# Kernel optimization log

Measured on AMD Instinct MI355X. Metric: run time of the kernel, lower is better.

## Reference

```python
import jax, jax.numpy as jnp
import numpy as np

B, H, W, D, L, M = 16, 256, 256, 32, 4, 12  # batch, grid H, grid W, d_model, num_layers, modes
BN_EPS = 1e-5


def setup_inputs() -> dict:
    key = jax.random.key(0)
    ks = jax.random.split(key, 12)
    scale = 1.0 / (D * D)  # SpectralConv2d init scale: 1/(in_ch*out_ch)
    return {
        "x": jax.random.normal(ks[0], (B, H, W), jnp.float32),
        "coords_x": jax.random.uniform(ks[1], (1, 2, 1, H, W), dtype=jnp.float32),
        # linear_in: 3 -> D
        "w_in": jax.random.normal(ks[2], (D, 3), jnp.float32) * 0.3,
        "b_in": jnp.zeros((D,), jnp.float32),
        # per-layer spectral weights (real/imag), torch.rand-style uniform [0,1)*scale
        "w1r": jax.random.uniform(ks[3], (L, D, D, M, M), dtype=jnp.float32) * scale,
        "w1i": jax.random.uniform(ks[4], (L, D, D, M, M), dtype=jnp.float32) * scale,
        "w2r": jax.random.uniform(ks[5], (L, D, D, M, M), dtype=jnp.float32) * scale,
        "w2i": jax.random.uniform(ks[6], (L, D, D, M, M), dtype=jnp.float32) * scale,
        # per-layer pointwise linear D -> D
        "lw": jax.random.normal(ks[7], (L, D, D), jnp.float32) * (1.0 / np.sqrt(D)),
        "lb": jnp.zeros((L, D), jnp.float32),
        # per-layer BatchNorm affine params
        "gamma": jnp.ones((L, D), jnp.float32),
        "beta": jnp.zeros((L, D), jnp.float32),
        # linear_out: D -> 1
        "w_out": jax.random.normal(ks[8], (1, D), jnp.float32) * (1.0 / np.sqrt(D)),
        "b_out": jnp.zeros((1,), jnp.float32),
    }


def _fourier_layer(h, w1, w2, lw, lb, gamma, beta):
    # h: [B, D, H, W]
    Bh, C, Hh, Wh = h.shape
    h_ft = jnp.fft.rfft2(h)  # [B, D, H, W//2+1] complex64
    # low-mode truncation + complex channel mixing on two corner blocks
    top = jnp.einsum('bixy,ioxy->boxy', h_ft[:, :, :M, :M], w1)
    bot = jnp.einsum('bixy,ioxy->boxy', h_ft[:, :, Hh - M:, :M], w2)
    out_ft = jnp.zeros((Bh, C, Hh, Wh // 2 + 1), jnp.complex64)
    out_ft = out_ft.at[:, :, :M, :M].set(top).at[:, :, Hh - M:, :M].set(bot)
    y = jnp.fft.irfft2(out_ft, s=(Hh, Wh))  # [B, D, H, W]
    # residual pointwise linear (x + Linear(x)), then ReLU, then BatchNorm2d (batch stats)
    y = y + jnp.einsum('bchw,oc->bohw', y, lw) + lb[None, :, None, None]
    y = jax.nn.relu(y)
    mean = y.mean(axis=(0, 2, 3), keepdims=True)
    var = y.var(axis=(0, 2, 3), keepdims=True)
    y = (y - mean) * jax.lax.rsqrt(var + BN_EPS)
    return y * gamma[None, :, None, None] + beta[None, :, None, None]


def reference(x, coords_x, w_in, b_in, w1r, w1i, w2r, w2i, lw, lb, gamma, beta, w_out, b_out):
    # coords_x: [1,2,1,H,W] -> squeeze dim 2 -> broadcast to [B,2,H,W]
    cx = jnp.broadcast_to(coords_x[:, :, 0], (x.shape[0], 2, H, W))
    h = jnp.concatenate([x[:, None], cx], axis=1)  # [B, 3, H, W]
    h = jnp.einsum('bchw,dc->bdhw', h, w_in) + b_in[None, :, None, None]  # linear_in
    for i in range(L):  # fixed small layer count
        h = _fourier_layer(h, w1r[i] + 1j * w1i[i], w2r[i] + 1j * w2i[i],
                           lw[i], lb[i], gamma[i], beta[i])
    out = jnp.einsum('bdhw,od->bohw', h, w_out) + b_out[None, :, None, None]  # linear_out
    return out[:, 0]  # [B, H, W]
```

## Files before the change

### kernel.cpp

```cpp
#include <hip/hip_runtime.h>

constexpr double PI2 = 6.283185307179586476925286766559;
constexpr float INV_HW = 1.0f / 65536.0f;


__global__ __launch_bounds__(256) void k_init(float* __restrict__ cs,
                                              float* __restrict__ Tg) {
  int t = threadIdx.x;
  double a = PI2 * (double)t / 256.0;
  cs[2*t]   = (float)cos(a);
  cs[2*t+1] = (float)sin(a);
  for (int i = t; i < 1536; i += 256) {
    int k = i >> 7, xs = i & 127;
    double ang = PI2 * (double)(k * xs) / 256.0;
    Tg[i]        = (float)cos(ang);
    Tg[1536 + i] = (float)sin(ang);
  }
  for (int i = t; i < 176; i += 256) {
    int k = (i >> 4) + 1, j = i & 15;
    double ang = PI2 * (double)(k * j) / 256.0;
    Tg[3072 + i] = (float)cos(ang);
    Tg[3248 + i] = (float)sin(ang);
  }
}

__global__ __launch_bounds__(256) void k_prep(
    const float* __restrict__ w1r, const float* __restrict__ w1i,
    const float* __restrict__ w2r, const float* __restrict__ w2i,
    const float* __restrict__ lw, float* __restrict__ wf)
{
  const int bid = blockIdx.x;
  const int l = bid / 288, m = bid % 288;
  const int ky = m / 12, kx = m % 12;
  const int kyp = (ky < 12) ? ky : ky - 12;
  const float* wr_ = ((ky < 12) ? w1r : w2r) + l*147456;
  const float* wi_ = ((ky < 12) ? w1i : w2i) + l*147456;
  __shared__ float wre[1024], wim[1024], lwl[1024];
  const int tid = threadIdx.x;
  for (int f = tid; f < 1024; f += 256) {
    int idx = f*144 + kyp*12 + kx;
    wre[f] = wr_[idx]; wim[f] = wi_[idx];
    lwl[f] = lw[l*1024 + f];
  }
  __syncthreads();
  float* o_ = wf + (long)bid*2048;
  for (int f = tid; f < 1024; f += 256) {
    int i = f >> 5, o = f & 31;
    float ar = wre[f], ai = wim[f];
    #pragma unroll
    for (int c = 0; c < 32; ++c) {
      float lv = lwl[o*32 + c];
      ar += wre[i*32 + c] * lv;
      ai += wim[i*32 + c] * lv;
    }
    o_[f] = ar; o_[1024 + f] = ai;
  }
}

__global__ __launch_bounds__(256) void k_embed_fwd(
    const float* __restrict__ xin, const float* __restrict__ coords,
    const float* __restrict__ w_in, const float* __restrict__ b_in,
    const float* __restrict__ Tg, float* __restrict__ gxo)
{
  __shared__ float wl[96], bl[32];
  __shared__ __align__(16) float Tl[3168];
  __shared__ __align__(16) float E[32*132];
  __shared__ __align__(16) float O[32*132];
  const int tid = threadIdx.x;
  if (tid < 96) wl[tid] = w_in[tid];
  if (tid >= 96 && tid < 128) bl[tid-96] = b_in[tid-96];
  for (int i = tid; i < 1536; i += 256) {
    int k = i >> 7, xs0 = i & 127;
    Tl[k*132 + xs0]        = Tg[i];
    Tl[1584 + k*132 + xs0] = Tg[1536 + i];
  }
  const int b = blockIdx.x >> 8, y = blockIdx.x & 255;
  const int xs = tid & 127, half = tid >> 7;
  const int cbase = half << 4;
  const int xhi = (256 - xs) & 255;
  const float xvL = xin[(b*256 + y)*256 + xs];
  const float c0L = coords[y*256 + xs];
  const float c1L = coords[65536 + y*256 + xs];
  const float xvH = xin[(b*256 + y)*256 + xhi];
  const float c0H = coords[y*256 + xhi];
  const float c1H = coords[65536 + y*256 + xhi];
  __syncthreads();
  #pragma unroll
  for (int cc = 0; cc < 16; ++cc) {
    const int c = cbase + cc;
    float lo = wl[3*c]*xvL + wl[3*c+1]*c0L + wl[3*c+2]*c1L + bl[c];
    float hi = wl[3*c]*xvH + wl[3*c+1]*c0H + wl[3*c+2]*c1H + bl[c];
    E[c*132 + xs] = (xs == 0) ? lo : (lo + hi);
    O[c*132 + xs] = (xs == 0) ? 0.f : (lo - hi);
  }
  if (tid < 32) {
    const int c = tid;
    const float xv = xin[(b*256 + y)*256 + 128];
    const float c0 = coords[y*256 + 128];
    const float c1 = coords[65536 + y*256 + 128];
    E[c*132 + 128] = wl[3*c]*xv + wl[3*c+1]*c0 + wl[3*c+2]*c1 + bl[c];
  }
  __syncthreads();
  const int wv = tid >> 6, lane = tid & 63;
  const int seg = lane >> 3, chl = lane & 7;
  const int ch = wv*8 + chl;
  float ar[12], ai[12];
  #pragma unroll
  for (int k = 0; k < 12; ++k) { ar[k] = 0.f; ai[k] = 0.f; }
  {
    const float* Erow = &E[ch*132 + seg*16];
    const float* Orow = &O[ch*132 + seg*16];
    #pragma unroll
    for (int c4 = 0; c4 < 4; ++c4) {
      float4 E4 = *(const float4*)(Erow + 4*c4);
      float4 O4 = *(const float4*)(Orow + 4*c4);
      ar[0] += E4.x + E4.y + E4.z + E4.w;
      #pragma unroll
      for (int k = 1; k < 12; ++k) {
        float4 Tc4 = *(const float4*)&Tl[k*132 + seg*16 + 4*c4];
        float4 Ts4 = *(const float4*)&Tl[1584 + k*132 + seg*16 + 4*c4];
        ar[k] += E4.x*Tc4.x + E4.y*Tc4.y + E4.z*Tc4.z + E4.w*Tc4.w;
        ai[k] -= O4.x*Ts4.x + O4.y*Ts4.y + O4.z*Ts4.z + O4.w*Ts4.w;
      }
    }
  }
  #pragma unroll
  for (int k = 0; k < 12; ++k) {
    ar[k] += __shfl_xor(ar[k], 8, 64);
    ar[k] += __shfl_xor(ar[k], 16, 64);
    ar[k] += __shfl_xor(ar[k], 32, 64);
  }
  #pragma unroll
  for (int k = 1; k < 12; ++k) {
    ai[k] += __shfl_xor(ai[k], 8, 64);
    ai[k] += __shfl_xor(ai[k], 16, 64);
    ai[k] += __shfl_xor(ai[k], 32, 64);
  }
  {
    const float e128 = E[ch*132 + 128];
    float* gp = gxo + ((long)(b*256 + y)*32 + ch)*24;
    #pragma unroll
    for (int j = 0; j < 3; ++j) {
      const int v = seg*3 + j;
      if (v < 12) {
        float s = ar[v] + ((v & 1) ? -e128 : e128);
        gp[2*v] = s;
        if (v == 0) gp[1] = 0.f;
      } else if (v < 23) {
        gp[2*(v - 11) + 1] = ai[v - 11];
      }
    }
  }
}

__global__ __launch_bounds__(512) void k_spec(
    const float* __restrict__ gx, const float* __restrict__ cs,
    const float* __restrict__ bnp, const float* __restrict__ wfl,
    float* __restrict__ gy)
{
  const int bid = (blockIdx.x % 8) * 24 + blockIdx.x / 8;
  const int b = bid / 12, kx = bid % 12;
  __shared__ float2 Z[32*257];
  __shared__ float fcl[24*66];
  __shared__ float fml[24*66];
  __shared__ __align__(16) float csl[512];
  const int tid = threadIdx.x;
  if (tid < 512) csl[tid] = cs[tid];
  {
    const int ch = tid & 31;
    float sc = 1.0f, badd = 0.0f;
    if (bnp) { sc = bnp[ch]; if (kx == 0) badd = 256.0f * bnp[32 + ch]; }
    const float* src = gx + ((long)(b*256)*32 + ch)*24 + 2*kx;
    const int ybase = tid >> 5;
    #pragma unroll
    for (int i = 0; i < 16; ++i) {
      int y = ybase + 16*i;
      float2 v = *(const float2*)(src + (long)y*768);
      float2 w; w.x = sc*v.x + badd; w.y = sc*v.y;
      Z[ch*257 + y] = w;
    }
  }
  __syncthreads();
  for (int t = tid; t < 832; t += 512) {
    const int hf = t & 1, r = t >> 1;
    const int pr = r % 13, ch = r / 13;
    const int kyv = (pr <= 10) ? (pr + 1) : ((pr == 11) ? 0 : 244);
    const int y0 = hf << 7;
    int tt = (kyv * y0) & 255;
    float A = 0.f, Bv = 0.f, C2 = 0.f, D = 0.f;
    const float2* Zp = &Z[ch*257 + y0];
    for (int i = 0; i < 128; ++i) {
      float2 v = Zp[i];
      float2 w = *(const float2*)&csl[2*tt];
      A  += v.x*w.x;  D  += v.x*w.y;
      C2 += v.y*w.x;  Bv += v.y*w.y;
      tt = (tt + kyv) & 255;
    }
    A  += __shfl_xor(A, 1, 64);
    Bv += __shfl_xor(Bv, 1, 64);
    C2 += __shfl_xor(C2, 1, 64);
    D  += __shfl_xor(D, 1, 64);
    if (hf == 0) {
      const int slo = (pr <= 10) ? (pr + 1) : ((pr == 11) ? 0 : 12);
      fcl[slo*66 + 2*ch]     = A + Bv;
      fcl[slo*66 + 2*ch + 1] = C2 - D;
      if (pr <= 10) {
        fcl[(23 - pr)*66 + 2*ch]     = A - Bv;
        fcl[(23 - pr)*66 + 2*ch + 1] = C2 + D;
      }
    }
  }
  __syncthreads();
  for (int t = tid; t < 768; t += 512) {
    const int ky = t >> 5, o = t & 31;
    const float* wb = wfl + ((long)(ky*12 + kx))*2048;
    const float* fr = &fcl[ky*66];
    float ar = 0.f, ai = 0.f;
    #pragma unroll
    for (int i = 0; i < 32; ++i) {
      float fre = fr[2*i], fim = fr[2*i+1];
      float wr = wb[i*32 + o], wi = wb[1024 + i*32 + o];
      ar += fre*wr - fim*wi;
      ai += fre*wi + fim*wr;
    }
    fml[ky*66 + 2*o]     = ar;
    fml[ky*66 + 2*o + 1] = ai;
  }
  __syncthreads();
  {
    const int yp = tid & 127, og = tid >> 7;
    float tc[24], tsn[24];
    #pragma unroll
    for (int s = 0; s < 24; ++s) {
      int kyv = (s < 12) ? s : (232 + s);
      int tt = (kyv * yp) & 255;
      tc[s] = csl[2*tt]; tsn[s] = csl[2*tt+1];
    }
    const int yhi = (256 - yp) & 255;
    float* rowLo = gy + ((long)(b*256 + yp))*768 + kx*64;
    float* rowHi = gy + ((long)(b*256 + yhi))*768 + kx*64;
    #pragma unroll
    for (int oo = 0; oo < 8; oo += 2) {
      const int o = og*8 + oo;
      float A1a=0.f,A2a=0.f,A3a=0.f,A4a=0.f;
      float A1b=0.f,A2b=0.f,A3b=0.f,A4b=0.f;
      #pragma unroll
      for (int s = 0; s < 24; ++s) {
        float fra = fml[s*66 + 2*o],     fia = fml[s*66 + 2*o + 1];
        float frb = fml[s*66 + 2*o + 2], fib = fml[s*66 + 2*o + 3];
        float c = tc[s], sn = tsn[s];
        A1a += fra*c;  A2a += fia*sn;  A3a += fra*sn;  A4a += fia*c;
        A1b += frb*c;  A2b += fib*sn;  A3b += frb*sn;  A4b += fib*c;
      }
      float4 lo, hi;
      lo.x = (A1a - A2a)*INV_HW; lo.y = (A3a + A4a)*INV_HW;
      lo.z = (A1b - A2b)*INV_HW; lo.w = (A3b + A4b)*INV_HW;
      hi.x = (A1a + A2a)*INV_HW; hi.y = (A4a - A3a)*INV_HW;
      hi.z = (A1b + A2b)*INV_HW; hi.w = (A4b - A3b)*INV_HW;
      *(float4*)(rowLo + 2*o) = lo;
      *(float4*)(rowHi + 2*o) = hi;
    }
  }
  if (tid < 32) {
    const int o = tid;
    float re = 0.f, im = 0.f;
    #pragma unroll
    for (int s = 0; s < 24; ++s) {
      float fr = fml[s*66 + 2*o], fi = fml[s*66 + 2*o + 1];
      if (s & 1) { re -= fr; im -= fi; } else { re += fr; im += fi; }
    }
    float* row = gy + ((long)(b*256 + 128))*768 + kx*64;
    row[2*o]     = re*INV_HW;
    row[2*o + 1] = im*INV_HW;
  }
}

__global__ __launch_bounds__(256) void k_fuse(
    const float* __restrict__ gy, const float* __restrict__ Tg,
    const float* __restrict__ lb,
    float* __restrict__ gxo, float* __restrict__ part, float* __restrict__ z)
{
  const int b = blockIdx.x >> 8, y = blockIdx.x & 255;
  const int tid = threadIdx.x;
  __shared__ __align__(16) float E[32*132];
  __shared__ __align__(16) float O[32*132];
  const int xs = tid & 127, half = tid >> 7;
  const int cbase = half << 4;
  const int xhi = (256 - xs) & 255;
  float tc[12], tsn[12];
  #pragma unroll
  for (int kx = 1; kx < 12; ++kx) {
    tc[kx]  = 2.0f * Tg[kx*128 + xs];
    tsn[kx] = 2.0f * Tg[1536 + kx*128 + xs];
  }
  const float* Gg = gy + (long)(b*256 + y)*768;
  float zlo[16], zhi[16];
  #pragma unroll
  for (int cc = 0; cc < 16; cc += 2) {
    const int c = cbase + cc;
    float base0 = Gg[2*c], base1 = Gg[2*c + 2];
    float cos0 = 0.f, sin0 = 0.f, cos1 = 0.f, sin1 = 0.f;
    #pragma unroll
    for (int kx = 1; kx < 12; ++kx) {
      float4 g = *(const float4*)(Gg + kx*64 + 2*c);
      cos0 += g.x*tc[kx];  sin0 += g.y*tsn[kx];
      cos1 += g.z*tc[kx];  sin1 += g.w*tsn[kx];
    }
    const float l0 = lb[c], l1 = lb[c+1];
    zlo[cc]   = fmaxf(base0 + cos0 - sin0 + l0, 0.f);
    zhi[cc]   = fmaxf(base0 + cos0 + sin0 + l0, 0.f);
    zlo[cc+1] = fmaxf(base1 + cos1 - sin1 + l1, 0.f);
    zhi[cc+1] = fmaxf(base1 + cos1 + sin1 + l1, 0.f);
  }
  #pragma unroll
  for (int cc = 0; cc < 16; ++cc) {
    float e = (xs == 0) ? zlo[cc] : (zlo[cc] + zhi[cc]);
    float o = (xs == 0) ? 0.f     : (zlo[cc] - zhi[cc]);
    E[(cbase+cc)*132 + xs] = e;
    O[(cbase+cc)*132 + xs] = o;
  }
  if (z) {
    #pragma unroll
    for (int cc = 0; cc < 16; ++cc) {
      z[((b*32 + cbase+cc)*256 + y)*256 + xs]  = zlo[cc];
      z[((b*32 + cbase+cc)*256 + y)*256 + xhi] = zhi[cc];
    }
  }
  if (tid < 32) {
    const int c = tid;
    float acc = Gg[2*c] + lb[c];
    #pragma unroll
    for (int kx = 1; kx < 12; ++kx) {
      float2 g = *(const float2*)(Gg + kx*64 + 2*c);
      acc += (kx & 1) ? (-2.0f * g.x) : (2.0f * g.x);
    }
    float zv = fmaxf(acc, 0.f);
    E[c*132 + 128] = zv;
    if (z) z[((b*32 + c)*256 + y)*256 + 128] = zv;
  }
  __syncthreads();
  const int wv = tid >> 6, lane = tid & 63;
  const int seg = lane >> 3, chl = lane & 7;
  const int ch = wv*8 + chl;
  const float* Erow = &E[ch*132 + seg*16];
  const float* Orow = &O[ch*132 + seg*16];
  float arr[12], aii[12], sq = 0.f;
  if (gxo) {
    const float* T2c = Tg + 3072;
    const float* T2s = Tg + 3248;
    float A[11], Bv[11], Cc[11], Dd[11];
    #pragma unroll
    for (int k = 0; k < 11; ++k) { A[k]=0.f; Bv[k]=0.f; Cc[k]=0.f; Dd[k]=0.f; }
    float s0 = 0.f;
    #pragma unroll
    for (int c4 = 0; c4 < 4; ++c4) {
      float4 E4 = *(const float4*)(Erow + 4*c4);
      float4 O4 = *(const float4*)(Orow + 4*c4);
      float ej[4] = {E4.x, E4.y, E4.z, E4.w};
      float oj[4] = {O4.x, O4.y, O4.z, O4.w};
      #pragma unroll
      for (int jj = 0; jj < 4; ++jj) {
        const int j = 4*c4 + jj;
        const float e = ej[jj], o = oj[jj];
        s0 += e;
        sq += e*e + o*o;
        #pragma unroll
        for (int k = 0; k < 11; ++k) {
          const float ckj = T2c[k*16 + j];
          const float skj = T2s[k*16 + j];
          A[k]  += e*ckj;
          Bv[k] += e*skj;
          Dd[k] += o*ckj;
          Cc[k] += o*skj;
        }
      }
    }
    arr[0] = s0; aii[0] = 0.f;
    #pragma unroll
    for (int k = 1; k < 12; ++k) {
      const float twc = Tg[k*128 + seg*16];
      const float tws = Tg[1536 + k*128 + seg*16];
      arr[k] = A[k-1]*twc - Bv[k-1]*tws;
      aii[k] = -(Cc[k-1]*twc + Dd[k-1]*tws);
    }
  } else {
    #pragma unroll
    for (int k = 0; k < 12; ++k) { arr[k]=0.f; aii[k]=0.f; }
    #pragma unroll
    for (int c4 = 0; c4 < 4; ++c4) {
      float4 E4 = *(const float4*)(Erow + 4*c4);
      float4 O4 = *(const float4*)(Orow + 4*c4);
      arr[0] += E4.x + E4.y + E4.z + E4.w;
      sq += E4.x*E4.x + E4.y*E4.y + E4.z*E4.z + E4.w*E4.w
          + O4.x*O4.x + O4.y*O4.y + O4.z*O4.z + O4.w*O4.w;
    }
  }
  #pragma unroll
  for (int k = 0; k < 12; ++k) {
    arr[k] += __shfl_xor(arr[k], 8, 64);
    arr[k] += __shfl_xor(arr[k], 16, 64);
    arr[k] += __shfl_xor(arr[k], 32, 64);
  }
  if (gxo) {
    #pragma unroll
    for (int k = 1; k < 12; ++k) {
      aii[k] += __shfl_xor(aii[k], 8, 64);
      aii[k] += __shfl_xor(aii[k], 16, 64);
      aii[k] += __shfl_xor(aii[k], 32, 64);
    }
  }
  sq += __shfl_xor(sq, 8, 64);
  sq += __shfl_xor(sq, 16, 64);
  sq += __shfl_xor(sq, 32, 64);
  {
    const float e0   = E[ch*132];
    const float e128 = E[ch*132 + 128];
    float* gp = gxo ? (gxo + ((long)(b*256 + y)*32 + ch)*24) : nullptr;
    #pragma unroll
    for (int j = 0; j < 3; ++j) {
      const int v = seg*3 + j;
      if (v < 12) {
        float s = arr[v] + ((v & 1) ? -e128 : e128);
        if (gp) {
          gp[2*v] = s;
          if (v == 0) gp[1] = 0.f;
        }
        if (v == 0) part[(long)blockIdx.x*64 + 2*ch] = s;
      } else if (v < 23) {
        if (gp) gp[2*(v - 11) + 1] = aii[v - 11];
      } else {
        part[(long)blockIdx.x*64 + 2*ch + 1] = 0.5f*sq + 0.5f*e0*e0 + e128*e128;
      }
    }
  }
}

__global__ __launch_bounds__(256) void k_stats(
    const float* __restrict__ part, const float* __restrict__ gamma,
    const float* __restrict__ beta, float* __restrict__ bn)
{
  const int c = blockIdx.x, tid = threadIdx.x;
  float s1 = 0.f, s2 = 0.f;
  for (int j = tid; j < 4096; j += 256) {
    s1 += part[(long)j*64 + 2*c];
    s2 += part[(long)j*64 + 2*c + 1];
  }
  #pragma unroll
  for (int d = 32; d; d >>= 1) {
    s1 += __shfl_xor(s1, d, 64);
    s2 += __shfl_xor(s2, d, 64);
  }
  __shared__ float r1[4], r2[4];
  int w = tid >> 6;
  if ((tid & 63) == 0) { r1[w] = s1; r2[w] = s2; }
  __syncthreads();
  if (tid == 0) {
    float S1 = r1[0]+r1[1]+r1[2]+r1[3];
    float S2 = r2[0]+r2[1]+r2[2]+r2[3];
    const float N = 1048576.0f;
    float mean = S1 / N;
    float var  = S2 / N - mean*mean;
    float inv  = rsqrtf(var + 1e-5f);
    float sc   = gamma[c] * inv;
    bn[c]      = sc;
    bn[32 + c] = beta[c] - mean*sc;
  }
}

__global__ __launch_bounds__(256) void k_out(
    const float* __restrict__ z, const float* __restrict__ bn,
    const float* __restrict__ w_out, const float* __restrict__ b_out,
    float* __restrict__ out)
{
  __shared__ float a[32];
  __shared__ float c0s;
  const int tid = threadIdx.x;
  if (tid < 32) a[tid] = bn[tid] * w_out[tid];
  if (tid == 0) {
    float t = b_out[0];
    for (int c = 0; c < 32; ++c) t += bn[32 + c] * w_out[c];
    c0s = t;
  }
  __syncthreads();
  int gid = blockIdx.x*256 + tid;
  int b = gid >> 14, pos = (gid & 16383) << 2;
  const float* zb = z + (long)b*2097152 + pos;
  float c0 = c0s;
  float r0 = c0, r1 = c0, r2 = c0, r3 = c0;
  #pragma unroll 8
  for (int c = 0; c < 32; ++c) {
    float4 v = *(const float4*)(zb + c*65536);
    float ac = a[c];
    r0 += v.x*ac; r1 += v.y*ac; r2 += v.z*ac; r3 += v.w*ac;
  }
  float4 res; res.x = r0; res.y = r1; res.z = r2; res.w = r3;
  *(float4*)(out + (long)b*65536 + pos) = res;
}

extern "C" void kernel_launch(void* const* d_in, const int* in_sizes, int n_in,
                              void* d_out, int out_size, void* d_ws, size_t ws_size,
                              hipStream_t stream) {
  const float* x      = (const float*)d_in[0];
  const float* coords = (const float*)d_in[1];
  const float* w_in   = (const float*)d_in[2];
  const float* b_in   = (const float*)d_in[3];
  const float* w1r    = (const float*)d_in[4];
  const float* w1i    = (const float*)d_in[5];
  const float* w2r    = (const float*)d_in[6];
  const float* w2i    = (const float*)d_in[7];
  const float* lw     = (const float*)d_in[8];
  const float* lb     = (const float*)d_in[9];
  const float* gamma  = (const float*)d_in[10];
  const float* beta   = (const float*)d_in[11];
  const float* w_out  = (const float*)d_in[12];
  const float* b_out  = (const float*)d_in[13];
  float* out = (float*)d_out;
  float* ws  = (float*)d_ws;

  float* cs   = ws;
  float* z    = cs + 512;
  float* gx   = z;
  float* wf   = z + 3145728;
  float* gy   = z + 33554432;
  float* part = gy + 3145728;
  float* Tg   = part + 294912;
  float* bn   = Tg + 294912;

  k_init<<<1, 256, 0, stream>>>(cs, Tg);
  k_prep<<<1152, 256, 0, stream>>>(w1r, w1i, w2r, w2i, lw, wf);
  k_embed_fwd<<<4096, 256, 0, stream>>>(x, coords, w_in, b_in, Tg, gx);

  for (int l = 0; l < 4; ++l) {
    k_spec<<<192, 512, 0, stream>>>(gx, cs, (l == 0) ? nullptr : bn,
                                    wf + (long)l*589824, gy);
    k_fuse<<<4096, 256, 0, stream>>>(gy, Tg, lb + l*32,
                                     (l < 3) ? gx : nullptr, part,
                                     (l == 3) ? z : nullptr);
    k_stats<<<32, 256, 0, stream>>>(part, gamma + l*32, beta + l*32, bn);
  }

  k_out<<<1024, 256, 0, stream>>>(z, bn, w_out, b_out, out);
}
```

Baseline: 486.0 us.

## Factor embed DFT into segment twiddles and double k_spec block threads

The embed forward kernel no longer stages the full 12x128 twiddle table in shared memory. It now accumulates against a small 11x16 local twiddle table read from global memory and applies a per-segment twiddle rotation afterwards, which trims shared-memory use and the staging loop. The spectral kernel moves from 512 to 1024 threads per block, splitting the y-DFT into quarters with an extra shuffle reduction and halving the per-thread output work in the inverse stage. This adds parallelism to a kernel that has only 192 blocks, at the cost of more shuffles and higher register pressure under the 1024-thread launch bound.

```diff
diff --git a/kernel.cpp b/kernel.cpp
--- a/kernel.cpp
+++ b/kernel.cpp
@@ -63,17 +63,11 @@
     const float* __restrict__ Tg, float* __restrict__ gxo)
 {
   __shared__ float wl[96], bl[32];
-  __shared__ __align__(16) float Tl[3168];
   __shared__ __align__(16) float E[32*132];
   __shared__ __align__(16) float O[32*132];
   const int tid = threadIdx.x;
   if (tid < 96) wl[tid] = w_in[tid];
   if (tid >= 96 && tid < 128) bl[tid-96] = b_in[tid-96];
-  for (int i = tid; i < 1536; i += 256) {
-    int k = i >> 7, xs0 = i & 127;
-    Tl[k*132 + xs0]        = Tg[i];
-    Tl[1584 + k*132 + xs0] = Tg[1536 + i];
-  }
   const int b = blockIdx.x >> 8, y = blockIdx.x & 255;
   const int xs = tid & 127, half = tid >> 7;
   const int cbase = half << 4;
@@ -104,37 +98,56 @@
   const int wv = tid >> 6, lane = tid & 63;
   const int seg = lane >> 3, chl = lane & 7;
   const int ch = wv*8 + chl;
-  float ar[12], ai[12];
-  #pragma unroll
-  for (int k = 0; k < 12; ++k) { ar[k] = 0.f; ai[k] = 0.f; }
-  {
-    const float* Erow = &E[ch*132 + seg*16];
-    const float* Orow = &O[ch*132 + seg*16];
-    #pragma unroll
-    for (int c4 = 0; c4 < 4; ++c4) {
-      float4 E4 = *(const float4*)(Erow + 4*c4);
-      float4 O4 = *(const float4*)(Orow + 4*c4);
-      ar[0] += E4.x + E4.y + E4.z + E4.w;
+  const float* Erow = &E[ch*132 + seg*16];
+  const float* Orow = &O[ch*132 + seg*16];
+  const float* T2c = Tg + 3072;
+  const float* T2s = Tg + 3248;
+  float A[11], Bv[11], Cc[11], Dd[11];
+  #pragma unroll
+  for (int k = 0; k < 11; ++k) { A[k]=0.f; Bv[k]=0.f; Cc[k]=0.f; Dd[k]=0.f; }
+  float s0 = 0.f;
+  #pragma unroll
+  for (int c4 = 0; c4 < 4; ++c4) {
+    float4 E4 = *(const float4*)(Erow + 4*c4);
+    float4 O4 = *(const float4*)(Orow + 4*c4);
+    float ej[4] = {E4.x, E4.y, E4.z, E4.w};
+    float oj[4] = {O4.x, O4.y, O4.z, O4.w};
+    #pragma unroll
+    for (int jj = 0; jj < 4; ++jj) {
+      const int j = 4*c4 + jj;
+      const float e = ej[jj], o = oj[jj];
+      s0 += e;
       #pragma unroll
-      for (int k = 1; k < 12; ++k) {
-        float4 Tc4 = *(const float4*)&Tl[k*132 + seg*16 + 4*c4];
-        float4 Ts4 = *(const float4*)&Tl[1584 + k*132 + seg*16 + 4*c4];
-        ar[k] += E4.x*Tc4.x + E4.y*Tc4.y + E4.z*Tc4.z + E4.w*Tc4.w;
-        ai[k] -= O4.x*Ts4.x + O4.y*Ts4.y + O4.z*Ts4.z + O4.w*Ts4.w;
+      for (int k = 0; k < 11; ++k) {
+        const float ckj = T2c[k*16 + j];
+        const float skj = T2s[k*16 + j];
+        A[k]  += e*ckj;
+        Bv[k] += e*skj;
+        Dd[k] += o*ckj;
+        Cc[k] += o*skj;
       }
     }
   }
+  float arr[12], aii[12];
+  arr[0] = s0; aii[0] = 0.f;
+  #pragma unroll
+  for (int k = 1; k < 12; ++k) {
+    const float twc = Tg[k*128 + seg*16];
+    const float tws = Tg[1536 + k*128 + seg*16];
+    arr[k] = A[k-1]*twc - Bv[k-1]*tws;
+    aii[k] = -(Cc[k-1]*twc + Dd[k-1]*tws);
+  }
   #pragma unroll
   for (int k = 0; k < 12; ++k) {
-    ar[k] += __shfl_xor(ar[k], 8, 64);
-    ar[k] += __shfl_xor(ar[k], 16, 64);
-    ar[k] += __shfl_xor(ar[k], 32, 64);
+    arr[k] += __shfl_xor(arr[k], 8, 64);
+    arr[k] += __shfl_xor(arr[k], 16, 64);
+    arr[k] += __shfl_xor(arr[k], 32, 64);
   }
   #pragma unroll
   for (int k = 1; k < 12; ++k) {
-    ai[k] += __shfl_xor(ai[k], 8, 64);
-    ai[k] += __shfl_xor(ai[k], 16, 64);
-    ai[k] += __shfl_xor(ai[k], 32, 64);
+    aii[k] += __shfl_xor(aii[k], 8, 64);
+    aii[k] += __shfl_xor(aii[k], 16, 64);
+    aii[k] += __shfl_xor(aii[k], 32, 64);
   }
   {
     const float e128 = E[ch*132 + 128];
@@ -143,17 +156,17 @@
     for (int j = 0; j < 3; ++j) {
       const int v = seg*3 + j;
       if (v < 12) {
-        float s = ar[v] + ((v & 1) ? -e128 : e128);
+        float s = arr[v] + ((v & 1) ? -e128 : e128);
         gp[2*v] = s;
         if (v == 0) gp[1] = 0.f;
       } else if (v < 23) {
-        gp[2*(v - 11) + 1] = ai[v - 11];
+        gp[2*(v - 11) + 1] = aii[v - 11];
       }
     }
   }
 }
 
-__global__ __launch_bounds__(512) void k_spec(
+__global__ __launch_bounds__(1024) void k_spec(
     const float* __restrict__ gx, const float* __restrict__ cs,
     const float* __restrict__ bnp, const float* __restrict__ wfl,
     float* __restrict__ gy)
@@ -173,23 +186,23 @@
     const float* src = gx + ((long)(b*256)*32 + ch)*24 + 2*kx;
     const int ybase = tid >> 5;
     #pragma unroll
-    for (int i = 0; i < 16; ++i) {
-      int y = ybase + 16*i;
+    for (int i = 0; i < 8; ++i) {
+      int y = ybase + 32*i;
       float2 v = *(const float2*)(src + (long)y*768);
       float2 w; w.x = sc*v.x + badd; w.y = sc*v.y;
       Z[ch*257 + y] = w;
     }
   }
   __syncthreads();
-  for (int t = tid; t < 832; t += 512) {
-    const int hf = t & 1, r = t >> 1;
+  for (int t = tid; t < 1664; t += 1024) {
+    const int qf = t & 3, r = t >> 2;
     const int pr = r % 13, ch = r / 13;
     const int kyv = (pr <= 10) ? (pr + 1) : ((pr == 11) ? 0 : 244);
-    const int y0 = hf << 7;
+    const int y0 = qf << 6;
     int tt = (kyv * y0) & 255;
     float A = 0.f, Bv = 0.f, C2 = 0.f, D = 0.f;
     const float2* Zp = &Z[ch*257 + y0];
-    for (int i = 0; i < 128; ++i) {
+    for (int i = 0; i < 64; ++i) {
       float2 v = Zp[i];
       float2 w = *(const float2*)&csl[2*tt];
       A  += v.x*w.x;  D  += v.x*w.y;
@@ -200,7 +213,11 @@
     Bv += __shfl_xor(Bv, 1, 64);
     C2 += __shfl_xor(C2, 1, 64);
     D  += __shfl_xor(D, 1, 64);
-    if (hf == 0) {
+    A  += __shfl_xor(A, 2, 64);
+    Bv += __shfl_xor(Bv, 2, 64);
+    C2 += __shfl_xor(C2, 2, 64);
+    D  += __shfl_xor(D, 2, 64);
+    if (qf == 0) {
       const int slo = (pr <= 10) ? (pr + 1) : ((pr == 11) ? 0 : 12);
       fcl[slo*66 + 2*ch]     = A + Bv;
       fcl[slo*66 + 2*ch + 1] = C2 - D;
@@ -211,8 +228,8 @@
     }
   }
   __syncthreads();
-  for (int t = tid; t < 768; t += 512) {
-    const int ky = t >> 5, o = t & 31;
+  if (tid < 768) {
+    const int ky = tid >> 5, o = tid & 31;
     const float* wb = wfl + ((long)(ky*12 + kx))*2048;
     const float* fr = &fcl[ky*66];
     float ar = 0.f, ai = 0.f;
@@ -240,8 +257,8 @@
     float* rowLo = gy + ((long)(b*256 + yp))*768 + kx*64;
     float* rowHi = gy + ((long)(b*256 + yhi))*768 + kx*64;
     #pragma unroll
-    for (int oo = 0; oo < 8; oo += 2) {
-      const int o = og*8 + oo;
+    for (int oo = 0; oo < 4; oo += 2) {
+      const int o = og*4 + oo;
       float A1a=0.f,A2a=0.f,A3a=0.f,A4a=0.f;
       float A1b=0.f,A2b=0.f,A3b=0.f,A4b=0.f;
       #pragma unroll
@@ -531,8 +548,8 @@
   k_embed_fwd<<<4096, 256, 0, stream>>>(x, coords, w_in, b_in, Tg, gx);
 
   for (int l = 0; l < 4; ++l) {
-    k_spec<<<192, 512, 0, stream>>>(gx, cs, (l == 0) ? nullptr : bn,
-                                    wf + (long)l*589824, gy);
+    k_spec<<<192, 1024, 0, stream>>>(gx, cs, (l == 0) ? nullptr : bn,
+                                     wf + (long)l*589824, gy);
     k_fuse<<<4096, 256, 0, stream>>>(gy, Tg, lb + l*32,
                                      (l < 3) ? gx : nullptr, part,
                                      (l == 3) ? z : nullptr);
```

New measurement: 507.6 us. 4.4% more time.
